# Performance work log

Hardware: AMD Instinct MI355X
Metric: run time of the kernel (lower is better)

Reference implementation:

```python
import jax, jax.numpy as jnp
import numpy as np

B, H, C = 1, 4, 32
D = H * C          # 128
S, L = 128, 256
EPS = 1e-5


def _axial_layer_norm(x, gamma, beta):
    # normalize over channel axis (axis=1) of [B, D, S, L]
    mu = jnp.mean(x, axis=1, keepdims=True)
    var = jnp.var(x, axis=1, keepdims=True)
    xn = (x - mu) * jax.lax.rsqrt(var + EPS)
    return xn * gamma[None, :, None, None] + beta[None, :, None, None]


def setup_inputs() -> dict:
    key = jax.random.key(0)
    ks = jax.random.split(key, 5)
    x = jax.random.normal(ks[0], (B, D, S, L), dtype=jnp.float32)
    w_row = jax.random.normal(ks[1], (3 * D, D), dtype=jnp.float32) * 0.02
    b_row = jax.random.normal(ks[2], (3 * D,), dtype=jnp.float32) * 0.02
    w_col = jax.random.normal(ks[3], (3 * D, D), dtype=jnp.float32) * 0.02
    b_col = jax.random.normal(ks[4], (3 * D,), dtype=jnp.float32) * 0.02
    return {
        "x": x,
        "w_row": w_row, "b_row": b_row,
        "w_col": w_col, "b_col": b_col,
        "gamma1": jnp.ones((D,), jnp.float32), "beta1": jnp.zeros((D,), jnp.float32),
        "gamma2": jnp.ones((D,), jnp.float32), "beta2": jnp.zeros((D,), jnp.float32),
    }


def _qkv(x, w, b):
    # 1x1 conv == channel matmul: [3D, D] x [B, D, S, L] -> [B, 3D, S, L]
    qkv = jnp.einsum('od,bdsl->bosl', w, x) + b[None, :, None, None]
    q, k, v = jnp.split(qkv, 3, axis=1)
    rs = lambda t: t.reshape(t.shape[0], H, C, S, L)
    return rs(q), rs(k), rs(v)


def reference(x, w_row, b_row, w_col, b_col, gamma1, beta1, gamma2, beta2):
    # --- row attention (attend along L within each row s) ---
    q, k, v = _qkv(x, w_row, b_row)
    row_attn = jnp.einsum('bhcsi,bhcsj->bhsij', q, k)   # [B,H,S,L,L], no 1/sqrt(d) scaling (as in source)
    row_attn = jax.nn.softmax(row_attn, axis=-1)
    row_out = jnp.einsum('bhsij,bhdsj->bhdsi', row_attn, v).reshape(x.shape[0], D, S, L)
    out = _axial_layer_norm(x + row_out, gamma1, beta1)

    # --- column attention (attend along S within each column l) ---
    q, k, v = _qkv(out, w_col, b_col)
    col_attn = jnp.einsum('bhcil,bhcjl->bhijl', q, k)   # [B,H,S,S,L]
    col_attn = jax.nn.softmax(col_attn, axis=-2)
    col_out = jnp.einsum('bhijl,bhdjl->bhdil', col_attn, v).reshape(x.shape[0], D, S, L)
    out = _axial_layer_norm(out + col_out, gamma2, beta2)
    return out
```

## Files before the change

kernel.cpp:

```cpp
#include <hip/hip_runtime.h>
#include <hip/hip_bf16.h>

#define SL     32768
#define EPS_LN 1e-5f

typedef unsigned short u16;
typedef __attribute__((ext_vector_type(8))) short bf16x8;
typedef __attribute__((ext_vector_type(4))) float f32x4;

#define MFMA16(a, b, c) __builtin_amdgcn_mfma_f32_16x16x32_bf16((a), (b), (c), 0, 0, 0)

__device__ inline u16 f2bf(float f) {
    __hip_bfloat16 h = __float2bfloat16(f);
    return *reinterpret_cast<u16*>(&h);
}
__device__ inline float bf2f(u16 u) {
    unsigned v = ((unsigned)u) << 16;
    float f;
    __builtin_memcpy(&f, &v, 4);
    return f;
}
__device__ inline uint4 pack8(float4 a, float4 b) {
    union { uint4 v; u16 u[8]; } U;
    U.u[0] = f2bf(a.x); U.u[1] = f2bf(a.y); U.u[2] = f2bf(a.z); U.u[3] = f2bf(a.w);
    U.u[4] = f2bf(b.x); U.u[5] = f2bf(b.y); U.u[6] = f2bf(b.z); U.u[7] = f2bf(b.w);
    return U.v;
}

__global__ __launch_bounds__(256) void wcast_kernel(const float* __restrict__ wr,
                                                    const float* __restrict__ wc,
                                                    u16* __restrict__ wrb,
                                                    u16* __restrict__ wcb) {
    const int i = blockIdx.x * 256 + threadIdx.x;
    const int NW = 384 * 128 / 8;
    const float* src = (i < NW) ? wr : wc;
    u16* dst = (i < NW) ? wrb : wcb;
    const int j = (i < NW) ? i : i - NW;
    float4 a = ((const float4*)src)[j * 2];
    float4 b = ((const float4*)src)[j * 2 + 1];
    ((uint4*)dst)[j] = pack8(a, b);
}

template<int LAYOUT>
__global__ __launch_bounds__(256) void qkv_mfma(const void* __restrict__ inv,
                                                const u16* __restrict__ wb,
                                                const float* __restrict__ bq,
                                                u16* __restrict__ qT,
                                                u16* __restrict__ kT,
                                                u16* __restrict__ vb) {
    __shared__ u16 xT[64][136];
    __shared__ float bs[128];
    const int bid = blockIdx.x;
    const int ot = bid % 3;
    const int o0 = ot * 128;
    const int n0 = (bid / 3) * 64;
    const int t = threadIdx.x;
    const int lane = t & 63, wv = t >> 6, lo = lane & 15, hi = lane >> 4;

    bf16x8 af[2][4];
    #pragma unroll
    for (int om = 0; om < 2; ++om)
        #pragma unroll
        for (int ks = 0; ks < 4; ++ks)
            af[om][ks] = *(const bf16x8*)(wb + (size_t)(o0 + wv * 32 + om * 16 + lo) * 128
                                             + hi * 8 + ks * 32);

    if constexpr (LAYOUT == 0) {
        #pragma unroll
        for (int itr = 0; itr < 4; ++itr) {
            const int u = t + itr * 256;
            const int d = u & 127, noct = u >> 7;
            const float* src = (const float*)inv + (size_t)d * SL + n0 + noct * 8;
            float4 f0 = *(const float4*)src;
            float4 f1 = *(const float4*)(src + 4);
            xT[noct * 8 + 0][d] = f2bf(f0.x);
            xT[noct * 8 + 1][d] = f2bf(f0.y);
            xT[noct * 8 + 2][d] = f2bf(f0.z);
            xT[noct * 8 + 3][d] = f2bf(f0.w);
            xT[noct * 8 + 4][d] = f2bf(f1.x);
            xT[noct * 8 + 5][d] = f2bf(f1.y);
            xT[noct * 8 + 6][d] = f2bf(f1.z);
            xT[noct * 8 + 7][d] = f2bf(f1.w);
        }
    } else {
        #pragma unroll
        for (int itr = 0; itr < 4; ++itr) {
            const int u = t + itr * 256;
            const int n = u >> 4, seg = u & 15;
            *(uint4*)&xT[n][seg * 8] =
                *(const uint4*)((const u16*)inv + (size_t)(n0 + n) * 128 + seg * 8);
        }
    }
    if (t < 128) bs[t] = bq[o0 + t];
    __syncthreads();

    u16* tbuf = (ot == 0) ? qT : kT;

    #pragma unroll
    for (int nt = 0; nt < 4; ++nt) {
        bf16x8 bfr[4];
        #pragma unroll
        for (int ks = 0; ks < 4; ++ks)
            bfr[ks] = *(const bf16x8*)&xT[nt * 16 + lo][hi * 8 + ks * 32];
        #pragma unroll
        for (int om = 0; om < 2; ++om) {
            f32x4 acc = {0.f, 0.f, 0.f, 0.f};
            #pragma unroll
            for (int ks = 0; ks < 4; ++ks)
                acc = MFMA16(af[om][ks], bfr[ks], acc);
            if (ot < 2) {
                ushort4 o4;
                o4.x = f2bf(acc[0] + bs[wv * 32 + om * 16 + hi * 4 + 0]);
                o4.y = f2bf(acc[1] + bs[wv * 32 + om * 16 + hi * 4 + 1]);
                o4.z = f2bf(acc[2] + bs[wv * 32 + om * 16 + hi * 4 + 2]);
                o4.w = f2bf(acc[3] + bs[wv * 32 + om * 16 + hi * 4 + 3]);
                *(ushort4*)(tbuf + (size_t)wv * SL * 32
                            + (size_t)(n0 + nt * 16 + lo) * 32 + om * 16 + hi * 4) = o4;
            } else {
                #pragma unroll
                for (int r = 0; r < 4; ++r) {
                    const int o = wv * 32 + om * 16 + hi * 4 + r;
                    vb[(size_t)o * SL + n0 + nt * 16 + lo] = f2bf(acc[r] + bs[o]);
                }
            }
        }
    }
}

template<int KLEN, int NTHR>
__global__ __launch_bounds__(NTHR) void attn_kernel(const u16* __restrict__ qT,
                                                    const u16* __restrict__ kT,
                                                    const u16* __restrict__ vb,
                                                    u16* __restrict__ ao) {
    constexpr int NJT = KLEN / 16;
    constexpr int NW = NTHR / 64;
    constexpr int NOUT = SL / KLEN;
    __shared__ u16 PT[NW][2][16][36];

    const int bid = blockIdx.x;
    const int outer = bid % NOUT;
    const int h = bid / NOUT;
    const int base = outer * KLEN;
    const int t = threadIdx.x;
    const int lane = t & 63, wv = t >> 6, lo = lane & 15, hi = lane >> 4;
    const int i0w = wv * 32;

    const u16* qh = qT + (size_t)h * SL * 32;
    const u16* kh = kT + (size_t)h * SL * 32;
    const u16* vh = vb + (size_t)h * 32 * SL;

    bf16x8 qf0 = *(const bf16x8*)(qh + (size_t)(base + i0w + lo) * 32 + hi * 8);
    bf16x8 qf1 = *(const bf16x8*)(qh + (size_t)(base + i0w + 16 + lo) * 32 + hi * 8);

    f32x4 o00 = {0.f, 0.f, 0.f, 0.f}, o01 = {0.f, 0.f, 0.f, 0.f};
    f32x4 o10 = {0.f, 0.f, 0.f, 0.f}, o11 = {0.f, 0.f, 0.f, 0.f};
    float ls0[4] = {0.f, 0.f, 0.f, 0.f};
    float ls1[4] = {0.f, 0.f, 0.f, 0.f};

    #pragma unroll
    for (int jt = 0; jt < NJT; ++jt) {
        bf16x8 kf = *(const bf16x8*)(kh + (size_t)(base + jt * 16 + lo) * 32 + hi * 8);
        f32x4 z = {0.f, 0.f, 0.f, 0.f};
        f32x4 s0 = MFMA16(qf0, kf, z);
        f32x4 s1 = MFMA16(qf1, kf, z);
        #pragma unroll
        for (int r = 0; r < 4; ++r) {
            float p0 = __expf(s0[r]);
            ls0[r] += p0;
            PT[wv][0][hi * 4 + r][(jt & 1) * 16 + lo] = f2bf(p0);
            float p1 = __expf(s1[r]);
            ls1[r] += p1;
            PT[wv][1][hi * 4 + r][(jt & 1) * 16 + lo] = f2bf(p1);
        }
        if (jt & 1) {
            const int jb = (jt - 1) * 16;
            bf16x8 pf0 = *(const bf16x8*)&PT[wv][0][lo][hi * 8];
            bf16x8 pf1 = *(const bf16x8*)&PT[wv][1][lo][hi * 8];
            bf16x8 v0 = *(const bf16x8*)(vh + (size_t)lo * SL + base + jb + hi * 8);
            bf16x8 v1 = *(const bf16x8*)(vh + (size_t)(16 + lo) * SL + base + jb + hi * 8);
            o00 = MFMA16(pf0, v0, o00);
            o01 = MFMA16(pf0, v1, o01);
            o10 = MFMA16(pf1, v0, o10);
            o11 = MFMA16(pf1, v1, o11);
        }
    }
    #pragma unroll
    for (int r = 0; r < 4; ++r) {
        float v0 = ls0[r];
        v0 += __shfl_xor(v0, 1);
        v0 += __shfl_xor(v0, 2);
        v0 += __shfl_xor(v0, 4);
        v0 += __shfl_xor(v0, 8);
        ls0[r] = 1.f / v0;
        float v1 = ls1[r];
        v1 += __shfl_xor(v1, 1);
        v1 += __shfl_xor(v1, 2);
        v1 += __shfl_xor(v1, 4);
        v1 += __shfl_xor(v1, 8);
        ls1[r] = 1.f / v1;
    }
    {
        ushort4 o4;
        o4.x = f2bf(o00[0] * ls0[0]);
        o4.y = f2bf(o00[1] * ls0[1]);
        o4.z = f2bf(o00[2] * ls0[2]);
        o4.w = f2bf(o00[3] * ls0[3]);
        *(ushort4*)(ao + (size_t)(h * 32 + lo) * SL + base + i0w + hi * 4) = o4;
        o4.x = f2bf(o01[0] * ls0[0]);
        o4.y = f2bf(o01[1] * ls0[1]);
        o4.z = f2bf(o01[2] * ls0[2]);
        o4.w = f2bf(o01[3] * ls0[3]);
        *(ushort4*)(ao + (size_t)(h * 32 + 16 + lo) * SL + base + i0w + hi * 4) = o4;
        o4.x = f2bf(o10[0] * ls1[0]);
        o4.y = f2bf(o10[1] * ls1[1]);
        o4.z = f2bf(o10[2] * ls1[2]);
        o4.w = f2bf(o10[3] * ls1[3]);
        *(ushort4*)(ao + (size_t)(h * 32 + lo) * SL + base + i0w + 16 + hi * 4) = o4;
        o4.x = f2bf(o11[0] * ls1[0]);
        o4.y = f2bf(o11[1] * ls1[1]);
        o4.z = f2bf(o11[2] * ls1[2]);
        o4.w = f2bf(o11[3] * ls1[3]);
        *(ushort4*)(ao + (size_t)(h * 32 + 16 + lo) * SL + base + i0w + 16 + hi * 4) = o4;
    }
}

__global__ __launch_bounds__(256) void ln_mid(const float* __restrict__ in0,
                                              const u16* __restrict__ in1,
                                              const float* __restrict__ g,
                                              const float* __restrict__ be,
                                              u16* __restrict__ outp) {
    __shared__ float val[128][69];
    __shared__ float redS[4][72];
    __shared__ float redQ[4][72];
    __shared__ float stat[64][2];
    __shared__ float gs[128], bes[128];
    const int bid = blockIdx.x;
    const int r0 = (bid / 16) * 4;
    const int c0 = (bid % 16) * 16;
    const int t = threadIdx.x;
    const int pos = t & 63, q = t >> 6;
    const size_t gp = (size_t)(r0 + (pos >> 4)) * 256 + c0 + (pos & 15);

    if (t < 128) { gs[t] = g[t]; bes[t] = be[t]; }
    float s = 0.f, ss = 0.f;
    #pragma unroll 4
    for (int dd = 0; dd < 32; ++dd) {
        const int d = q * 32 + dd;
        float v = in0[(size_t)d * SL + gp] + bf2f(in1[(size_t)d * SL + gp]);
        val[d][pos] = v;
        s += v; ss += v * v;
    }
    redS[q][pos] = s;
    redQ[q][pos] = ss;
    __syncthreads();
    if (t < 64) {
        const float S  = redS[0][t] + redS[1][t] + redS[2][t] + redS[3][t];
        const float SS = redQ[0][t] + redQ[1][t] + redQ[2][t] + redQ[3][t];
        const float mean = S * (1.f / 128.f);
        const float var  = SS * (1.f / 128.f) - mean * mean;
        stat[t][0] = mean;
        stat[t][1] = rsqrtf(var + EPS_LN);
    }
    __syncthreads();

    {
        const int pr = pos >> 4, pc = pos & 15;
        const size_t pp = (size_t)(c0 + pc) * 128 + r0 + pr;
        const float mean = stat[pos][0], rstd = stat[pos][1];
        union { uint4 v[4]; u16 u[32]; } O;
        #pragma unroll
        for (int dd = 0; dd < 32; ++dd) {
            const int d = q * 32 + dd;
            O.u[dd] = f2bf((val[d][pos] - mean) * rstd * gs[d] + bes[d]);
        }
        uint4* dst = (uint4*)(outp + pp * 128 + q * 32);
        #pragma unroll
        for (int k = 0; k < 4; ++k) dst[k] = O.v[k];
    }
}

__global__ __launch_bounds__(256) void ln_out(const u16* __restrict__ in0,
                                              const u16* __restrict__ in1,
                                              const float* __restrict__ g,
                                              const float* __restrict__ be,
                                              float* __restrict__ outp) {
    __shared__ float val[128][69];
    __shared__ float redS[4][72];
    __shared__ float redQ[4][72];
    __shared__ float stat[64][2];
    const int bid = blockIdx.x;
    const int r0 = (bid / 8) * 4;
    const int c0 = (bid % 8) * 16;
    const int t = threadIdx.x;
    const int pos = t & 63, q = t >> 6;
    const size_t gp = (size_t)(r0 + (pos >> 4)) * 128 + c0 + (pos & 15);

    float s = 0.f, ss = 0.f;
    {
        union { uint4 v[4]; u16 u[32]; } A;
        const uint4* src = (const uint4*)(in0 + gp * 128 + q * 32);
        #pragma unroll
        for (int k = 0; k < 4; ++k) A.v[k] = src[k];
        #pragma unroll 4
        for (int dd = 0; dd < 32; ++dd) {
            const int d = q * 32 + dd;
            float v = bf2f(A.u[dd]) + bf2f(in1[(size_t)d * SL + gp]);
            val[d][pos] = v;
            s += v; ss += v * v;
        }
    }
    redS[q][pos] = s;
    redQ[q][pos] = ss;
    __syncthreads();
    if (t < 64) {
        const float S  = redS[0][t] + redS[1][t] + redS[2][t] + redS[3][t];
        const float SS = redQ[0][t] + redQ[1][t] + redQ[2][t] + redQ[3][t];
        const float mean = S * (1.f / 128.f);
        const float var  = SS * (1.f / 128.f) - mean * mean;
        stat[t][0] = mean;
        stat[t][1] = rsqrtf(var + EPS_LN);
    }
    __syncthreads();

    {
        const int d = t >> 1;
        const int ch = (t & 1) * 8;
        const float gd = g[d], bd = be[d];
        #pragma unroll
        for (int cc = 0; cc < 8; ++cc) {
            const int c = ch + cc;
            float ov[4];
            #pragma unroll
            for (int r = 0; r < 4; ++r) {
                const int p = r * 16 + c;
                ov[r] = (val[d][p] - stat[p][0]) * stat[p][1] * gd + bd;
            }
            float* dst = outp + (size_t)d * SL + (c0 + c) * 256 + r0;
            *(float4*)dst = make_float4(ov[0], ov[1], ov[2], ov[3]);
        }
    }
}

extern "C" void kernel_launch(void* const* d_in, const int* in_sizes, int n_in,
                              void* d_out, int out_size, void* d_ws, size_t ws_size,
                              hipStream_t stream) {
    const float* x     = (const float*)d_in[0];
    const float* w_row = (const float*)d_in[1];
    const float* b_row = (const float*)d_in[2];
    const float* w_col = (const float*)d_in[3];
    const float* b_col = (const float*)d_in[4];
    const float* g1    = (const float*)d_in[5];
    const float* be1   = (const float*)d_in[6];
    const float* g2    = (const float*)d_in[7];
    const float* be2   = (const float*)d_in[8];
    float* out = (float*)d_out;

    char* base = (char*)d_ws;
    u16* qTb = (u16*)base;                        base += (size_t)128 * SL * 2;
    u16* kTb = (u16*)base;                        base += (size_t)128 * SL * 2;
    u16* vbb = (u16*)base;                        base += (size_t)128 * SL * 2;
    u16* ao16 = (u16*)base;                       base += (size_t)128 * SL * 2;
    u16* o1b  = (u16*)base;                       base += (size_t)128 * SL * 2;
    u16* wrb  = (u16*)base;                       base += (size_t)384 * 128 * 2;
    u16* wcb  = (u16*)base;

    wcast_kernel<<<48, 256, 0, stream>>>(w_row, w_col, wrb, wcb);
    qkv_mfma<0><<<1536, 256, 0, stream>>>(x, wrb, b_row, qTb, kTb, vbb);
    attn_kernel<256, 512><<<512, 512, 0, stream>>>(qTb, kTb, vbb, ao16);
    ln_mid<<<512, 256, 0, stream>>>(x, ao16, g1, be1, o1b);
    qkv_mfma<1><<<1536, 256, 0, stream>>>(o1b, wcb, b_col, qTb, kTb, vbb);
    attn_kernel<128, 256><<<1024, 256, 0, stream>>>(qTb, kTb, vbb, ao16);
    ln_out<<<512, 256, 0, stream>>>(o1b, ao16, g2, be2, out);
}
```

Before: 101.6 us.

## Compute all Q, K and V for a column tile in one QKV block

The QKV projection kernel previously launched three blocks per 64-column tile, one for each of Q, K and V, and each block reloaded and transposed the same input tile. Now one 512-thread block (8 waves, 48 output rows each) computes all 384 output channels for its tile, so the input is read and converted once instead of three times. The trade-off is one third as many blocks, more weight-fragment registers per wave, and mixed Q/K/V store paths inside a wave's output range.

```diff
diff --git a/kernel.cpp b/kernel.cpp
--- a/kernel.cpp
+++ b/kernel.cpp
@@ -42,33 +42,24 @@
 }
 
 template<int LAYOUT>
-__global__ __launch_bounds__(256) void qkv_mfma(const void* __restrict__ inv,
+__global__ __launch_bounds__(512) void qkv_mfma(const void* __restrict__ inv,
                                                 const u16* __restrict__ wb,
                                                 const float* __restrict__ bq,
                                                 u16* __restrict__ qT,
                                                 u16* __restrict__ kT,
                                                 u16* __restrict__ vb) {
     __shared__ u16 xT[64][136];
-    __shared__ float bs[128];
-    const int bid = blockIdx.x;
-    const int ot = bid % 3;
-    const int o0 = ot * 128;
-    const int n0 = (bid / 3) * 64;
+    __shared__ float bs[384];
+    const int n0 = blockIdx.x * 64;
     const int t = threadIdx.x;
     const int lane = t & 63, wv = t >> 6, lo = lane & 15, hi = lane >> 4;
 
-    bf16x8 af[2][4];
-    #pragma unroll
-    for (int om = 0; om < 2; ++om)
-        #pragma unroll
-        for (int ks = 0; ks < 4; ++ks)
-            af[om][ks] = *(const bf16x8*)(wb + (size_t)(o0 + wv * 32 + om * 16 + lo) * 128
-                                             + hi * 8 + ks * 32);
+    if (t < 384) bs[t] = bq[t];
 
     if constexpr (LAYOUT == 0) {
         #pragma unroll
-        for (int itr = 0; itr < 4; ++itr) {
-            const int u = t + itr * 256;
+        for (int itr = 0; itr < 2; ++itr) {
+            const int u = t + itr * 512;
             const int d = u & 127, noct = u >> 7;
             const float* src = (const float*)inv + (size_t)d * SL + n0 + noct * 8;
             float4 f0 = *(const float4*)src;
@@ -84,44 +75,53 @@
         }
     } else {
         #pragma unroll
-        for (int itr = 0; itr < 4; ++itr) {
-            const int u = t + itr * 256;
+        for (int itr = 0; itr < 2; ++itr) {
+            const int u = t + itr * 512;
             const int n = u >> 4, seg = u & 15;
             *(uint4*)&xT[n][seg * 8] =
                 *(const uint4*)((const u16*)inv + (size_t)(n0 + n) * 128 + seg * 8);
         }
     }
-    if (t < 128) bs[t] = bq[o0 + t];
-    __syncthreads();
-
-    u16* tbuf = (ot == 0) ? qT : kT;
+    __syncthreads();
+
+    bf16x8 af[3][4];
+    #pragma unroll
+    for (int om = 0; om < 3; ++om)
+        #pragma unroll
+        for (int ks = 0; ks < 4; ++ks)
+            af[om][ks] = *(const bf16x8*)(wb + (size_t)(wv * 48 + om * 16 + lo) * 128
+                                             + hi * 8 + ks * 32);
 
     #pragma unroll
     for (int nt = 0; nt < 4; ++nt) {
+        const int n = n0 + nt * 16 + lo;
         bf16x8 bfr[4];
         #pragma unroll
         for (int ks = 0; ks < 4; ++ks)
             bfr[ks] = *(const bf16x8*)&xT[nt * 16 + lo][hi * 8 + ks * 32];
         #pragma unroll
-        for (int om = 0; om < 2; ++om) {
+        for (int om = 0; om < 3; ++om) {
+            const int obase = wv * 48 + om * 16;
             f32x4 acc = {0.f, 0.f, 0.f, 0.f};
             #pragma unroll
             for (int ks = 0; ks < 4; ++ks)
                 acc = MFMA16(af[om][ks], bfr[ks], acc);
-            if (ot < 2) {
+            if (obase < 256) {
+                u16* tbuf = (obase < 128) ? qT : kT;
+                const int ob = obase & 127;
+                const int h = ob >> 5;
+                const int cb = (ob & 31) + hi * 4;
                 ushort4 o4;
-                o4.x = f2bf(acc[0] + bs[wv * 32 + om * 16 + hi * 4 + 0]);
-                o4.y = f2bf(acc[1] + bs[wv * 32 + om * 16 + hi * 4 + 1]);
-                o4.z = f2bf(acc[2] + bs[wv * 32 + om * 16 + hi * 4 + 2]);
-                o4.w = f2bf(acc[3] + bs[wv * 32 + om * 16 + hi * 4 + 3]);
-                *(ushort4*)(tbuf + (size_t)wv * SL * 32
-                            + (size_t)(n0 + nt * 16 + lo) * 32 + om * 16 + hi * 4) = o4;
+                o4.x = f2bf(acc[0] + bs[obase + hi * 4 + 0]);
+                o4.y = f2bf(acc[1] + bs[obase + hi * 4 + 1]);
+                o4.z = f2bf(acc[2] + bs[obase + hi * 4 + 2]);
+                o4.w = f2bf(acc[3] + bs[obase + hi * 4 + 3]);
+                *(ushort4*)(tbuf + (size_t)h * SL * 32 + (size_t)n * 32 + cb) = o4;
             } else {
+                const int orow = obase - 256 + hi * 4;
                 #pragma unroll
-                for (int r = 0; r < 4; ++r) {
-                    const int o = wv * 32 + om * 16 + hi * 4 + r;
-                    vb[(size_t)o * SL + n0 + nt * 16 + lo] = f2bf(acc[r] + bs[o]);
-                }
+                for (int r = 0; r < 4; ++r)
+                    vb[(size_t)(orow + r) * SL + n] = f2bf(acc[r] + bs[obase + hi * 4 + r]);
             }
         }
     }
@@ -365,10 +365,10 @@
     u16* wcb  = (u16*)base;
 
     wcast_kernel<<<48, 256, 0, stream>>>(w_row, w_col, wrb, wcb);
-    qkv_mfma<0><<<1536, 256, 0, stream>>>(x, wrb, b_row, qTb, kTb, vbb);
+    qkv_mfma<0><<<512, 512, 0, stream>>>(x, wrb, b_row, qTb, kTb, vbb);
     attn_kernel<256, 512><<<512, 512, 0, stream>>>(qTb, kTb, vbb, ao16);
     ln_mid<<<512, 256, 0, stream>>>(x, ao16, g1, be1, o1b);
-    qkv_mfma<1><<<1536, 256, 0, stream>>>(o1b, wcb, b_col, qTb, kTb, vbb);
+    qkv_mfma<1><<<512, 512, 0, stream>>>(o1b, wcb, b_col, qTb, kTb, vbb);
     attn_kernel<128, 256><<<1024, 256, 0, stream>>>(qTb, kTb, vbb, ao16);
     ln_out<<<512, 256, 0, stream>>>(o1b, ao16, g2, be2, out);
 }
```

After: 98.70 us. -2.9%, faster.
